# Kernel tuning notes

Measured on AMD Instinct MI355X. Metric: run time of the kernel, lower is better.

## Reference

```python
import jax, jax.numpy as jnp
import numpy as np
from jax import lax

RADIUS = 0.15
K = 32          # num_neighbors
S = 1024        # num_centers
GROUPS = 8      # GroupNorm groups
EPS = 1e-5


def furthest_point_sample(xyz, n_samples):
    # xyz: [B, N, 3] -> indices [B, n_samples] (sequential FPS, start at index 0)
    B, N, _ = xyz.shape
    def step(carry, _):
        min_d, far = carry                      # [B,N], [B]
        sel = jnp.take_along_axis(xyz, far[:, None, None], axis=1)  # [B,1,3]
        d = jnp.sum((xyz - sel) ** 2, axis=-1)  # [B,N]
        min_d = jnp.minimum(min_d, d)
        nxt = jnp.argmax(min_d, axis=-1).astype(jnp.int32)
        return (min_d, nxt), far
    init = (jnp.full((B, N), jnp.inf, dtype=xyz.dtype), jnp.zeros((B,), jnp.int32))
    _, idxs = lax.scan(step, init, None, length=n_samples)  # [n_samples, B]
    return idxs.T  # [B, n_samples]


def ball_query(centers, points, radius, k):
    # centers: [B,3,S], points: [B,3,N] -> neighbor indices [B,S,k]
    B = points.shape[0]
    N = points.shape[-1]
    d2 = jnp.sum((centers[:, :, :, None] - points[:, :, None, :]) ** 2, axis=1)  # [B,S,N]
    valid = d2 < radius * radius
    order = jnp.where(valid, jnp.arange(N, dtype=jnp.int32), jnp.int32(N))
    topk = jnp.sort(order, axis=-1)[..., :k]            # first-k in-ball indices (CUDA ball_query order)
    first = topk[..., :1]
    idx = jnp.where(topk < N, topk, first)              # pad shortfall with first in-ball point
    idx = jnp.where(idx == N, 0, idx)                   # empty ball -> index 0
    return idx


def grouping(x, idx):
    # x: [B,C,N], idx: [B,S,k] -> [B,C,S,k]
    B, C, N = x.shape
    _, s, k = idx.shape
    flat = idx.reshape(B, 1, s * k)
    g = jnp.take_along_axis(x, jnp.broadcast_to(flat, (B, C, s * k)), axis=2)
    return g.reshape(B, C, s, k)


def group_norm(x, gamma, beta):
    # x: [B,C,S,K], GroupNorm(GROUPS)
    B, C, s, k = x.shape
    xg = x.reshape(B, GROUPS, C // GROUPS, s, k)
    mu = jnp.mean(xg, axis=(2, 3, 4), keepdims=True)
    var = jnp.var(xg, axis=(2, 3, 4), keepdims=True)
    xn = ((xg - mu) * lax.rsqrt(var + EPS)).reshape(B, C, s, k)
    return xn * gamma[None, :, None, None] + beta[None, :, None, None]


def mlp_layer(x, w, b, gamma, beta):
    # 1x1 Conv2d + GroupNorm + swish; x: [B,C,S,K], w: [O,C]
    y = jnp.einsum('bcsk,oc->bosk', x, w) + b[None, :, None, None]
    y = group_norm(y, gamma, beta)
    return y * jax.nn.sigmoid(y)


def setup_inputs() -> dict:
    key = jax.random.key(0)
    ks = jax.random.split(key, 20)
    B, C_IN, N = 8, 128, 4096
    features = jax.random.normal(ks[0], (B, C_IN, N), jnp.float32)
    coords = jax.random.uniform(ks[1], (B, 3, N), jnp.float32)
    time_emb = jax.random.normal(ks[2], (B, 64, N), jnp.float32)
    style = jax.random.normal(ks[3], (B, 64), jnp.float32)
    chans = [C_IN + 3, 128, 128, 256]
    inp = dict(features=features, coords=coords, time_emb=time_emb, style=style)
    for i in range(3):
        ci, co = chans[i], chans[i + 1]
        inp[f'w{i+1}'] = jax.random.normal(ks[4 + 4 * i], (co, ci), jnp.float32) / np.sqrt(ci)
        inp[f'b{i+1}'] = jnp.zeros((co,), jnp.float32)
        inp[f'g{i+1}'] = jnp.ones((co,), jnp.float32)
        inp[f'be{i+1}'] = jnp.zeros((co,), jnp.float32)
    return inp


def reference(features, coords, time_emb, style,
              w1, b1, g1, be1, w2, b2, g2, be2, w3, b3, g3, be3):
    # FPS -> center coords
    fps_idx = furthest_point_sample(coords.transpose(0, 2, 1), S)       # [B,S]
    B = coords.shape[0]
    centers = jnp.take_along_axis(coords, jnp.broadcast_to(fps_idx[:, None, :], (B, 3, S)), axis=2)  # [B,3,S]
    # Ball query + grouping (include_coordinates=True)
    nidx = ball_query(centers, coords, RADIUS, K)                       # [B,S,K]
    ncoords = grouping(coords, nidx) - centers[:, :, :, None]           # [B,3,S,K]
    nfeat = jnp.concatenate([ncoords, grouping(features, nidx)], axis=1)  # [B,3+C,S,K]
    # SharedMLP (1x1 conv + GN(8) + swish) x3, then max over neighbors
    x = mlp_layer(nfeat, w1, b1, g1, be1)
    x = mlp_layer(x, w2, b2, g2, be2)
    x = mlp_layer(x, w3, b3, g3, be3)
    out = jnp.max(x, axis=-1)                                           # [B,256,S]
    return out, centers, time_emb[:, :, :S], style
```

## Files before the change

kernel.cpp:

```cpp
#include <hip/hip_runtime.h>
#include <hip/hip_bf16.h>

#define BATCH 8
#define NPTS 4096
#define NS   1024
#define NK   32
#define CIN  128
#define C1PAD 160
#define O1   128
#define O3   256
#define MTOT 32768
#define GN_EPS 1e-5f

typedef float f32x4 __attribute__((ext_vector_type(4)));
typedef float f32x2 __attribute__((ext_vector_type(2)));
typedef short s16x8 __attribute__((ext_vector_type(8)));
typedef short s16x4 __attribute__((ext_vector_type(4)));
typedef unsigned long long u64;
typedef u64 u64x2 __attribute__((ext_vector_type(2)));

static __device__ __forceinline__ unsigned short f2bf(float f){
  unsigned u = __float_as_uint(f);
  u += 0x7fffu + ((u >> 16) & 1u);
  return (unsigned short)(u >> 16);
}
static __device__ __forceinline__ float bf2f(unsigned short h){
  return __uint_as_float(((unsigned)h) << 16);
}
static __device__ __forceinline__ float exact_d2(float ax,float ay,float az,float bx,float by,float bz){
  float dx=__fadd_rn(ax,-bx), dy=__fadd_rn(ay,-by), dz=__fadd_rn(az,-bz);
  return __fadd_rn(__fadd_rn(__fmul_rn(dx,dx),__fmul_rn(dy,dy)),__fmul_rn(dz,dz));
}
static __device__ __forceinline__ unsigned wave_umax_dpp(unsigned v){
  unsigned o;
  o = (unsigned)__builtin_amdgcn_update_dpp(0, (int)v, 0x111, 0xf, 0xf, true); v = (o>v)?o:v;
  o = (unsigned)__builtin_amdgcn_update_dpp(0, (int)v, 0x112, 0xf, 0xf, true); v = (o>v)?o:v;
  o = (unsigned)__builtin_amdgcn_update_dpp(0, (int)v, 0x114, 0xf, 0xf, true); v = (o>v)?o:v;
  o = (unsigned)__builtin_amdgcn_update_dpp(0, (int)v, 0x118, 0xf, 0xf, true); v = (o>v)?o:v;
  o = (unsigned)__builtin_amdgcn_update_dpp(0, (int)v, 0x142, 0xf, 0xf, true); v = (o>v)?o:v;
  o = (unsigned)__builtin_amdgcn_update_dpp(0, (int)v, 0x143, 0xf, 0xf, true); v = (o>v)?o:v;
  return v;
}
static __device__ __forceinline__ float wave_fsum_dpp(float v){
  int o;
  o=__builtin_amdgcn_update_dpp(0,__float_as_int(v),0x111,0xf,0xf,true); v+=__int_as_float(o);
  o=__builtin_amdgcn_update_dpp(0,__float_as_int(v),0x112,0xf,0xf,true); v+=__int_as_float(o);
  o=__builtin_amdgcn_update_dpp(0,__float_as_int(v),0x114,0xf,0xf,true); v+=__int_as_float(o);
  o=__builtin_amdgcn_update_dpp(0,__float_as_int(v),0x118,0xf,0xf,true); v+=__int_as_float(o);
  o=__builtin_amdgcn_update_dpp(0,__float_as_int(v),0x142,0xf,0xf,true); v+=__int_as_float(o);
  o=__builtin_amdgcn_update_dpp(0,__float_as_int(v),0x143,0xf,0xf,true); v+=__int_as_float(o);
  return v;
}
static __device__ __forceinline__ float fast_sigmoid(float x){
  return __builtin_amdgcn_rcpf(1.0f + __expf(-x));
}

#define FPS_BLOCKS 8
#define FT_BASE    8
#define FT_BLOCKS  128
#define ZP_BASE    136
#define ZP_BLOCKS  8
#define WP_BASE    144
#define WP_BLOCKS  36
#define MS_BASE    180
#define MS_BLOCKS  32
#define TOTAL_BLOCKS 212

__global__ __launch_bounds__(256) void k_fused(
    const float* __restrict__ coords, const float* __restrict__ features,
    const float* __restrict__ time_emb, const float* __restrict__ style,
    const float* __restrict__ w1, const float* __restrict__ w2, const float* __restrict__ w3,
    float* __restrict__ centers, float* __restrict__ out_time, float* __restrict__ out_style,
    unsigned short* __restrict__ featT, unsigned short* __restrict__ wfrag,
    float* __restrict__ stats){
  union U {
    struct { float4 lc[NPTS];
             unsigned long long red[2][4] __attribute__((aligned(16))); } fps;
    float tile[64][65];
  };
  __shared__ U sm;
  const int blk = blockIdx.x;
  const int t = threadIdx.x;

  if(blk < FPS_BLOCKS){
    const int b = blk;
    const float* cb = coords + (size_t)b*3*NPTS;
    const int lane = t & 63, wid = t >> 6;
    f32x2 px2[8],py2[8],pz2[8],md2[8];
    #pragma unroll
    for(int i=0;i<8;++i){
      int p0 = t + (2*i)*256;
      px2[i]=(f32x2){cb[p0],cb[p0+256]};
      py2[i]=(f32x2){cb[NPTS+p0],cb[NPTS+p0+256]};
      pz2[i]=(f32x2){cb[2*NPTS+p0],cb[2*NPTS+p0+256]};
      md2[i]=(f32x2){3.4e38f,3.4e38f};
      sm.fps.lc[p0]     = make_float4(px2[i].x, py2[i].x, pz2[i].x, 0.f);
      sm.fps.lc[p0+256] = make_float4(px2[i].y, py2[i].y, pz2[i].y, 0.f);
    }
    float ax=cb[0], ay=cb[NPTS], az=cb[2*NPTS];
    if(t==0){
      centers[(size_t)(b*3+0)*NS]=ax;
      centers[(size_t)(b*3+1)*NS]=ay;
      centers[(size_t)(b*3+2)*NS]=az;
    }
    __syncthreads();
    for(int it=1; it<NS; ++it){
      {
        #pragma clang fp contract(off)
        f32x2 axv={ax,ax}, ayv={ay,ay}, azv={az,az};
        #pragma unroll
        for(int i=0;i<8;++i){
          f32x2 dx=px2[i]-axv, dy=py2[i]-ayv, dz=pz2[i]-azv;
          f32x2 d = dx*dx + dy*dy + dz*dz;
          md2[i].x=fminf(md2[i].x,d.x);
          md2[i].y=fminf(md2[i].y,d.y);
        }
      }
      float m[8];
      #pragma unroll
      for(int i=0;i<8;++i) m[i]=fmaxf(md2[i].x,md2[i].y);
      float bmax=fmaxf(fmaxf(fmaxf(m[0],m[1]),fmaxf(m[2],m[3])),
                       fmaxf(fmaxf(m[4],m[5]),fmaxf(m[6],m[7])));
      unsigned bvb=(unsigned)__builtin_amdgcn_readlane((int)wave_umax_dpp(__float_as_uint(bmax)),63);
      unsigned cand=0u;
      #pragma unroll
      for(int s=15;s>=0;--s){
        float mv = (s&1)? md2[s>>1].y : md2[s>>1].x;
        cand = (__float_as_uint(mv)==bvb) ? ~(unsigned)(s*256+t) : cand;
      }
      unsigned mc = wave_umax_dpp(cand);
      const int buf=it&1;
      if(lane==63) sm.fps.red[buf][wid] = ((u64)bvb<<32) | mc;
      __syncthreads();
      u64x2 r0 = *(const u64x2*)&sm.fps.red[buf][0];
      u64x2 r1 = *(const u64x2*)&sm.fps.red[buf][2];
      u64 a0 = r0.x>r0.y?r0.x:r0.y;
      u64 a1 = r1.x>r1.y?r1.x:r1.y;
      u64 w  = a0>a1?a0:a1;
      unsigned idx = ~(unsigned)w;
      float4 c4 = sm.fps.lc[idx];
      ax=c4.x; ay=c4.y; az=c4.z;
      if(t==0){
        centers[(size_t)(b*3+0)*NS+it]=ax;
        centers[(size_t)(b*3+1)*NS+it]=ay;
        centers[(size_t)(b*3+2)*NS+it]=az;
      }
    }
    return;
  }

  if(blk < ZP_BASE){
    const int pb = blk - FT_BASE;
    for(int j=0;j<8;++j){
      int tid = pb*8 + j;
      int bb = tid>>7, r = tid&127, ct = r>>6, pt = r&63;
      int c0 = ct*64, p0 = pt*64;
      #pragma unroll
      for(int i=0;i<16;++i){
        int c = (t>>6)*16 + i;
        sm.tile[c][t&63] = features[((size_t)bb*CIN + c0 + c)*NPTS + p0 + (t&63)];
      }
      __syncthreads();
      #pragma unroll
      for(int i=0;i<16;++i){
        int pl = (t>>6)*16 + i;
        featT[((size_t)bb*NPTS + p0 + pl)*C1PAD + c0 + (t&63)] = f2bf(sm.tile[t&63][pl]);
      }
      __syncthreads();
    }
    return;
  }

  if(blk < WP_BASE){
    const int zb = blk - ZP_BASE;
    s16x8 z = (s16x8){0,0,0,0,0,0,0,0};
    #pragma unroll 4
    for(int i=0;i<64;++i){
      int q = zb*16384 + i*256 + t;
      int bb = q>>14, rem = q&16383, r = rem>>2, c8 = (rem&3)*8;
      *(s16x8*)&featT[((size_t)bb*NPTS + r)*C1PAD + 128 + c8] = z;
    }
    return;
  }

  if(blk < MS_BASE){
    int task = (blk - WP_BASE)*256 + t;
    if(task >= 9088) return;
    if(task >= 8704){
      int z = task - 8704;
      if(z < 3*BATCH*8*2) stats[z] = 0.f;
      return;
    }
    int layer, of, cs, ln, ncs; size_t base;
    if(task < 2560){ layer=0; ncs=5; base=0;     int r=task;      of=r/320; r%=320; cs=r>>6; ln=r&63; }
    else if(task < 4608){ layer=1; ncs=4; base=20480; int r=task-2560; of=r>>8; r&=255; cs=r>>6; ln=r&63; }
    else { layer=2; ncs=4; base=36864; int r=task-4608; of=r>>8; r&=255; cs=r>>6; ln=r&63; }
    int o = of*16 + (ln&15);
    s16x8 vals;
    #pragma unroll
    for(int i=0;i<8;++i){
      int c = cs*32 + (ln>>4)*8 + i;
      float v = 0.f;
      if(layer==0){
        if(c<128) v = w1[o*131 + c + 3];
        else if(c<131) v = w1[o*131 + (c-128)];
      } else if(layer==1){
        if(c<128) v = w2[o*128 + c];
      } else {
        if(c<128) v = w3[o*128 + c];
      }
      vals[i]=(short)f2bf(v);
    }
    *(s16x8*)&wfrag[base + ((size_t)(of*ncs + cs)*64 + ln)*8] = vals;
    return;
  }

  {
    const int mb = blk - MS_BASE;
    #pragma unroll 4
    for(int i=0;i<16;++i){
      int q = mb*4096 + i*256 + t;
      int f = q*4;
      int bb = f>>16, c = (f>>10)&63, s = f&1023;
      *(float4*)&out_time[f] = *(const float4*)&time_emb[((size_t)bb*64 + c)*NPTS + s];
    }
    if(mb==0){ out_style[t]=style[t]; out_style[256+t]=style[256+t]; }
  }
}

__global__ __launch_bounds__(256) void k_ballq(const float* __restrict__ coords,
                                               const float* __restrict__ centers,
                                               int* __restrict__ nidx){
  const int gw = (blockIdx.x*256 + threadIdx.x) >> 6;
  const int lane = threadIdx.x & 63;
  const int wl = (threadIdx.x >> 6);
  const int b = gw >> 10, s = gw & (NS-1);
  const float* cb = coords + (size_t)b*3*NPTS;
  const float cx = centers[(size_t)(b*3+0)*NS+s];
  const float cy = centers[(size_t)(b*3+1)*NS+s];
  const float cz = centers[(size_t)(b*3+2)*NS+s];
  __shared__ int slots[4][NK];
  int cnt = 0;
  for(int base=0; base<NPTS && cnt<NK; base+=64){
    int p = base + lane;
    float d2 = exact_d2(cb[p], cb[NPTS+p], cb[2*NPTS+p], cx,cy,cz);
    bool valid = d2 < 0.0225f;
    unsigned long long mask = __ballot(valid);
    int pos = cnt + (int)__popcll(mask & ((1ull<<lane)-1ull));
    if(valid && pos < NK) slots[wl][pos] = p;
    cnt += (int)__popcll(mask);
  }
  __syncthreads();
  int first = slots[wl][0];
  if(lane < NK){
    int v = (lane < cnt) ? slots[wl][lane] : first;
    nidx[((size_t)b*NS + s)*NK + lane] = v;
  }
}

__global__ __launch_bounds__(256) void k_gemm1(const unsigned short* __restrict__ featT,
    const int* __restrict__ nidx, const float* __restrict__ coords,
    const float* __restrict__ centers, const unsigned short* __restrict__ wfrag,
    const float* __restrict__ bias, unsigned short* __restrict__ yout,
    float* __restrict__ stats){
  const int b=blockIdx.y, mt=blockIdx.x;
  const int m0=mt*64;
  const int t=threadIdx.x, lane=t&63, wid=t>>6;
  __shared__ unsigned short xs[64][168];
  __shared__ unsigned short ys[64][136];
  __shared__ int pidx[64];
  __shared__ float cenS[2][3];
  __shared__ float wsum[2][8][4];
  if(t<64) pidx[t]=nidx[(size_t)b*MTOT + m0 + t];
  if(t>=64 && t<70){ int u=t-64; int j=u/3, c=u%3; cenS[j][c]=centers[((size_t)b*3+c)*NS + (m0>>5)+j]; }
  __syncthreads();
  for(int q=t;q<1280;q+=256){
    int r=q&63, ch=q>>6;
    *(s16x8*)&xs[r][ch*8] = *(const s16x8*)&featT[((size_t)b*NPTS + pidx[r])*C1PAD + ch*8];
  }
  __syncthreads();
  if(t<64){
    int p=pidx[t]; int sj=t>>5;
    float n0=__fadd_rn(coords[((size_t)b*3+0)*NPTS+p],-cenS[sj][0]);
    float n1=__fadd_rn(coords[((size_t)b*3+1)*NPTS+p],-cenS[sj][1]);
    float n2=__fadd_rn(coords[((size_t)b*3+2)*NPTS+p],-cenS[sj][2]);
    s16x4 nc={(short)f2bf(n0),(short)f2bf(n1),(short)f2bf(n2),0};
    *(s16x4*)&xs[t][128]=nc;
  }
  __syncthreads();
  f32x4 acc[8];
  #pragma unroll
  for(int i=0;i<8;++i) acc[i]=(f32x4){0.f,0.f,0.f,0.f};
  const unsigned short* xrow=&xs[wid*16+(lane&15)][0];
  #pragma unroll
  for(int cs=0;cs<5;++cs){
    s16x8 bfv=*(const s16x8*)&xrow[cs*32+(lane>>4)*8];
    #pragma unroll
    for(int of=0;of<8;++of){
      s16x8 afv=*(const s16x8*)&wfrag[((size_t)(of*5+cs)*64+lane)*8];
      acc[of]=__builtin_amdgcn_mfma_f32_16x16x32_bf16(afv,bfv,acc[of],0,0,0);
    }
  }
  #pragma unroll
  for(int of=0;of<8;++of){
    float ls=0.f,lq=0.f;
    int obase=of*16+((lane>>4)<<2);
    #pragma unroll
    for(int r=0;r<4;++r){
      float y=acc[of][r]+bias[obase+r];
      ys[wid*16+(lane&15)][obase+r]=f2bf(y);
      ls+=y; lq+=y*y;
    }
    ls=wave_fsum_dpp(ls); lq=wave_fsum_dpp(lq);
    if(lane==63){ wsum[0][of][wid]=ls; wsum[1][of][wid]=lq; }
  }
  __syncthreads();
  for(int q=t;q<1024;q+=256){
    int r=q&63, ch=q>>6;
    *(s16x8*)&yout[((size_t)b*MTOT+m0+r)*O1 + ch*8] = *(const s16x8*)&ys[r][ch*8];
  }
  if(t<8){
    float s1v=wsum[0][t][0]+wsum[0][t][1]+wsum[0][t][2]+wsum[0][t][3];
    float s2v=wsum[1][t][0]+wsum[1][t][1]+wsum[1][t][2]+wsum[1][t][3];
    atomicAdd(&stats[((0*BATCH+b)*8+t)*2+0],s1v);
    atomicAdd(&stats[((0*BATCH+b)*8+t)*2+1],s2v);
  }
}

template<int LAYER>
__global__ __launch_bounds__(256) void k_gemm23(const unsigned short* __restrict__ xin,
    const unsigned short* __restrict__ wfrag, const float* __restrict__ bias,
    const float* __restrict__ stats, const float* __restrict__ gprev,
    const float* __restrict__ beprev, unsigned short* __restrict__ yout,
    float* __restrict__ ymm, float* __restrict__ statsOut){
  const int b=blockIdx.y, mt=blockIdx.x;
  const int m0=mt*64;
  const int t=threadIdx.x, lane=t&63, wid=t>>6;
  __shared__ unsigned short xs[64][136];
  __shared__ unsigned short ys[64][136];
  __shared__ float lsc[CIN], lsh[CIN];
  __shared__ float wsum[2][8][4];
  if(t<CIN){
    int g = t>>4;
    const float cnt = 16.0f*NS*NK;
    float s1=stats[(((LAYER-1)*BATCH+b)*8+g)*2+0];
    float s2=stats[(((LAYER-1)*BATCH+b)*8+g)*2+1];
    float mu=s1/cnt, var=s2/cnt-mu*mu;
    float sc=gprev[t]*rsqrtf(var+GN_EPS);
    lsc[t]=sc; lsh[t]=beprev[t]-mu*sc;
  }
  __syncthreads();
  for(int q=t;q<1024;q+=256){
    int r=q&63, ch=q>>6;
    s16x8 v = *(const s16x8*)&xin[((size_t)b*MTOT + m0 + r)*CIN + ch*8];
    s16x8 o;
    #pragma unroll
    for(int i=0;i<8;++i){
      int c=ch*8+i;
      float x = bf2f((unsigned short)v[i]);
      x = x*lsc[c] + lsh[c];
      o[i]=(short)f2bf(x*fast_sigmoid(x));
    }
    *(s16x8*)&xs[r][ch*8]=o;
  }
  __syncthreads();
  const unsigned short* xrow=&xs[wid*16+(lane&15)][0];
  s16x8 bfv[4];
  #pragma unroll
  for(int cs=0;cs<4;++cs) bfv[cs]=*(const s16x8*)&xrow[cs*32+(lane>>4)*8];
  const int NPH=(LAYER==2)?2:1;
  #pragma unroll
  for(int ph=0; ph<NPH; ++ph){
    f32x4 acc[8];
    #pragma unroll
    for(int i=0;i<8;++i) acc[i]=(f32x4){0.f,0.f,0.f,0.f};
    #pragma unroll
    for(int cs=0;cs<4;++cs){
      #pragma unroll
      for(int of=0;of<8;++of){
        int ofg=ph*8+of;
        s16x8 afv=*(const s16x8*)&wfrag[((size_t)(ofg*4+cs)*64+lane)*8];
        acc[of]=__builtin_amdgcn_mfma_f32_16x16x32_bf16(afv,bfv[cs],acc[of],0,0,0);
      }
    }
    #pragma unroll
    for(int of=0;of<8;++of){
      float ls=0.f,lq=0.f;
      int lobase=of*16+((lane>>4)<<2);
      #pragma unroll
      for(int r=0;r<4;++r){
        float y=acc[of][r]+bias[ph*128+lobase+r];
        ys[wid*16+(lane&15)][lobase+r]=f2bf(y);
        ls+=y; lq+=y*y;
      }
      ls=wave_fsum_dpp(ls); lq=wave_fsum_dpp(lq);
      if(lane==63){ wsum[0][of][wid]=ls; wsum[1][of][wid]=lq; }
    }
    __syncthreads();
    if constexpr(LAYER==1){
      for(int q=t;q<1024;q+=256){
        int r=q&63, ch=q>>6;
        *(s16x8*)&yout[((size_t)b*MTOT+m0+r)*O1 + ch*8] = *(const s16x8*)&ys[r][ch*8];
      }
    } else {
      int c = t&127, sg = t>>7;
      float mn=3.4e38f, mx=-3.4e38f;
      #pragma unroll 8
      for(int k=0;k<32;++k){
        float v = bf2f(ys[sg*32+k][c]);
        mn=fminf(mn,v); mx=fmaxf(mx,v);
      }
      *(float2*)&ymm[(((size_t)b*NS + mt*2 + sg)*512) + (size_t)(ph*128+c)*2] = make_float2(mn,mx);
    }
    if(t<8){
      float s1v=wsum[0][t][0]+wsum[0][t][1]+wsum[0][t][2]+wsum[0][t][3];
      float s2v=wsum[1][t][0]+wsum[1][t][1]+wsum[1][t][2]+wsum[1][t][3];
      int g = (LAYER==2) ? (ph*4 + (t>>1)) : t;
      atomicAdd(&statsOut[((LAYER*BATCH+b)*8+g)*2+0],s1v);
      atomicAdd(&statsOut[((LAYER*BATCH+b)*8+g)*2+1],s2v);
    }
    if(ph+1<NPH) __syncthreads();
  }
}

__global__ __launch_bounds__(256) void k_out(const float* __restrict__ ymm,
    const float* __restrict__ stats, const float* __restrict__ g3,
    const float* __restrict__ be3, float* __restrict__ out){
  const int b=blockIdx.z, st=blockIdx.x;
  const int t=threadIdx.x;
  __shared__ float outT[256][33];
  const int c=t, g=c>>5;
  const float cnt = 32.0f*NS*NK;
  float s1=stats[((2*BATCH+b)*8+g)*2+0];
  float s2=stats[((2*BATCH+b)*8+g)*2+1];
  float mu=s1/cnt, var=s2/cnt-mu*mu;
  float sc=g3[c]*rsqrtf(var+GN_EPS);
  float sh=be3[c]-mu*sc;
  for(int si=0;si<32;++si){
    int s=st*32+si;
    float2 v=*(const float2*)&ymm[((size_t)b*NS+s)*512 + (size_t)c*2];
    float za=v.x*sc+sh, zb=v.y*sc+sh;
    float fa=za*fast_sigmoid(za);
    float fb=zb*fast_sigmoid(zb);
    outT[c][si]=fmaxf(fa,fb);
  }
  __syncthreads();
  #pragma unroll
  for(int i=0;i<32;++i){
    int row=(t>>5)+i*8;
    out[((size_t)(b*256+row))*NS + st*32 + (t&31)] = outT[row][t&31];
  }
}

extern "C" void kernel_launch(void* const* d_in, const int* in_sizes, int n_in,
                              void* d_out, int out_size, void* d_ws, size_t ws_size,
                              hipStream_t stream){
  const float* features=(const float*)d_in[0];
  const float* coords=(const float*)d_in[1];
  const float* time_emb=(const float*)d_in[2];
  const float* style=(const float*)d_in[3];
  const float* w1=(const float*)d_in[4];
  const float* b1=(const float*)d_in[5];
  const float* g1=(const float*)d_in[6];
  const float* be1=(const float*)d_in[7];
  const float* w2=(const float*)d_in[8];
  const float* b2=(const float*)d_in[9];
  const float* g2=(const float*)d_in[10];
  const float* be2=(const float*)d_in[11];
  const float* w3=(const float*)d_in[12];
  const float* b3=(const float*)d_in[13];
  const float* g3=(const float*)d_in[14];
  const float* be3=(const float*)d_in[15];

  float* out0=(float*)d_out;
  float* out_centers=out0 + (size_t)BATCH*O3*NS;
  float* out_time=out_centers + (size_t)BATCH*3*NS;
  float* out_style=out_time + (size_t)BATCH*64*NS;

  char* ws=(char*)d_ws;
  int* nidx=(int*)(ws + 131072);
  unsigned short* featT=(unsigned short*)(ws + 1179648);
  unsigned short* wfrag=(unsigned short*)(ws + 11796480);
  float* stats=(float*)(ws + 11939840);
  float* ymm=(float*)(ws + 12582912);
  unsigned short* y1=(unsigned short*)(ws + 33554432);
  unsigned short* y2=(unsigned short*)(ws + 100663296);

  k_fused<<<TOTAL_BLOCKS,256,0,stream>>>(coords,features,time_emb,style,w1,w2,w3,
                                         out_centers,out_time,out_style,featT,wfrag,stats);
  k_ballq<<<2048,256,0,stream>>>(coords,out_centers,nidx);
  k_gemm1<<<dim3(512,BATCH),256,0,stream>>>(featT,nidx,coords,out_centers,wfrag,b1,y1,stats);
  k_gemm23<1><<<dim3(512,BATCH),256,0,stream>>>(y1,wfrag+20480,b2,stats,g1,be1,y2,ymm,stats);
  k_gemm23<2><<<dim3(512,BATCH),256,0,stream>>>(y2,wfrag+36864,b3,stats,g2,be2,y2,ymm,stats);
  k_out<<<dim3(32,1,BATCH),256,0,stream>>>(ymm,stats,g3,be3,out0);
}
```

Baseline: 1.051 ms.

## Process two batches per FPS block to share per-iteration barrier latency

Each furthest-point-sampling block now handles two batch elements at once, which halves the FPS block count. The two independent dependency chains are interleaved in a single iteration loop with one __syncthreads. The aim is to hide the latency of the serial reduce-and-barrier chain by giving each wave twice the independent work. The cost is twice the registers and LDS per block and roughly double the ALU work per iteration, so each FPS block may run longer.

```diff
diff --git a/kernel.cpp b/kernel.cpp
--- a/kernel.cpp
+++ b/kernel.cpp
@@ -55,16 +55,16 @@
   return __builtin_amdgcn_rcpf(1.0f + __expf(-x));
 }
 
-#define FPS_BLOCKS 8
-#define FT_BASE    8
+#define FPS_BLOCKS 4
+#define FT_BASE    4
 #define FT_BLOCKS  128
-#define ZP_BASE    136
+#define ZP_BASE    132
 #define ZP_BLOCKS  8
-#define WP_BASE    144
+#define WP_BASE    140
 #define WP_BLOCKS  36
-#define MS_BASE    180
+#define MS_BASE    176
 #define MS_BLOCKS  32
-#define TOTAL_BLOCKS 212
+#define TOTAL_BLOCKS 208
 
 __global__ __launch_bounds__(256) void k_fused(
     const float* __restrict__ coords, const float* __restrict__ features,
@@ -74,8 +74,9 @@
     unsigned short* __restrict__ featT, unsigned short* __restrict__ wfrag,
     float* __restrict__ stats){
   union U {
-    struct { float4 lc[NPTS];
-             unsigned long long red[2][4] __attribute__((aligned(16))); } fps;
+    struct { float4 lcA[NPTS]; float4 lcB[NPTS];
+             unsigned long long redA[2][4] __attribute__((aligned(16)));
+             unsigned long long redB[2][4] __attribute__((aligned(16))); } fps;
     float tile[64][65];
   };
   __shared__ U sm;
@@ -83,67 +84,107 @@
   const int t = threadIdx.x;
 
   if(blk < FPS_BLOCKS){
-    const int b = blk;
-    const float* cb = coords + (size_t)b*3*NPTS;
+    const int bA = blk*2, bB = blk*2+1;
+    const float* cbA = coords + (size_t)bA*3*NPTS;
+    const float* cbB = coords + (size_t)bB*3*NPTS;
     const int lane = t & 63, wid = t >> 6;
-    f32x2 px2[8],py2[8],pz2[8],md2[8];
+    f32x2 pxA[8],pyA[8],pzA[8],mdA[8];
+    f32x2 pxB[8],pyB[8],pzB[8],mdB[8];
     #pragma unroll
     for(int i=0;i<8;++i){
       int p0 = t + (2*i)*256;
-      px2[i]=(f32x2){cb[p0],cb[p0+256]};
-      py2[i]=(f32x2){cb[NPTS+p0],cb[NPTS+p0+256]};
-      pz2[i]=(f32x2){cb[2*NPTS+p0],cb[2*NPTS+p0+256]};
-      md2[i]=(f32x2){3.4e38f,3.4e38f};
-      sm.fps.lc[p0]     = make_float4(px2[i].x, py2[i].x, pz2[i].x, 0.f);
-      sm.fps.lc[p0+256] = make_float4(px2[i].y, py2[i].y, pz2[i].y, 0.f);
-    }
-    float ax=cb[0], ay=cb[NPTS], az=cb[2*NPTS];
+      pxA[i]=(f32x2){cbA[p0],cbA[p0+256]};
+      pyA[i]=(f32x2){cbA[NPTS+p0],cbA[NPTS+p0+256]};
+      pzA[i]=(f32x2){cbA[2*NPTS+p0],cbA[2*NPTS+p0+256]};
+      pxB[i]=(f32x2){cbB[p0],cbB[p0+256]};
+      pyB[i]=(f32x2){cbB[NPTS+p0],cbB[NPTS+p0+256]};
+      pzB[i]=(f32x2){cbB[2*NPTS+p0],cbB[2*NPTS+p0+256]};
+      mdA[i]=(f32x2){3.4e38f,3.4e38f};
+      mdB[i]=(f32x2){3.4e38f,3.4e38f};
+      sm.fps.lcA[p0]     = make_float4(pxA[i].x, pyA[i].x, pzA[i].x, 0.f);
+      sm.fps.lcA[p0+256] = make_float4(pxA[i].y, pyA[i].y, pzA[i].y, 0.f);
+      sm.fps.lcB[p0]     = make_float4(pxB[i].x, pyB[i].x, pzB[i].x, 0.f);
+      sm.fps.lcB[p0+256] = make_float4(pxB[i].y, pyB[i].y, pzB[i].y, 0.f);
+    }
+    float axA=cbA[0], ayA=cbA[NPTS], azA=cbA[2*NPTS];
+    float axB=cbB[0], ayB=cbB[NPTS], azB=cbB[2*NPTS];
     if(t==0){
-      centers[(size_t)(b*3+0)*NS]=ax;
-      centers[(size_t)(b*3+1)*NS]=ay;
-      centers[(size_t)(b*3+2)*NS]=az;
+      centers[(size_t)(bA*3+0)*NS]=axA;
+      centers[(size_t)(bA*3+1)*NS]=ayA;
+      centers[(size_t)(bA*3+2)*NS]=azA;
+    } else if(t==1){
+      centers[(size_t)(bB*3+0)*NS]=axB;
+      centers[(size_t)(bB*3+1)*NS]=ayB;
+      centers[(size_t)(bB*3+2)*NS]=azB;
     }
     __syncthreads();
     for(int it=1; it<NS; ++it){
       {
         #pragma clang fp contract(off)
-        f32x2 axv={ax,ax}, ayv={ay,ay}, azv={az,az};
+        f32x2 axvA={axA,axA}, ayvA={ayA,ayA}, azvA={azA,azA};
+        f32x2 axvB={axB,axB}, ayvB={ayB,ayB}, azvB={azB,azB};
         #pragma unroll
         for(int i=0;i<8;++i){
-          f32x2 dx=px2[i]-axv, dy=py2[i]-ayv, dz=pz2[i]-azv;
-          f32x2 d = dx*dx + dy*dy + dz*dz;
-          md2[i].x=fminf(md2[i].x,d.x);
-          md2[i].y=fminf(md2[i].y,d.y);
+          f32x2 dxA=pxA[i]-axvA, dyA=pyA[i]-ayvA, dzA=pzA[i]-azvA;
+          f32x2 dA = dxA*dxA + dyA*dyA + dzA*dzA;
+          mdA[i]=__builtin_elementwise_min(mdA[i],dA);
+          f32x2 dxB=pxB[i]-axvB, dyB=pyB[i]-ayvB, dzB=pzB[i]-azvB;
+          f32x2 dB = dxB*dxB + dyB*dyB + dzB*dzB;
+          mdB[i]=__builtin_elementwise_min(mdB[i],dB);
         }
       }
-      float m[8];
-      #pragma unroll
-      for(int i=0;i<8;++i) m[i]=fmaxf(md2[i].x,md2[i].y);
-      float bmax=fmaxf(fmaxf(fmaxf(m[0],m[1]),fmaxf(m[2],m[3])),
-                       fmaxf(fmaxf(m[4],m[5]),fmaxf(m[6],m[7])));
-      unsigned bvb=(unsigned)__builtin_amdgcn_readlane((int)wave_umax_dpp(__float_as_uint(bmax)),63);
-      unsigned cand=0u;
+      f32x2 tA=__builtin_elementwise_max(
+                 __builtin_elementwise_max(__builtin_elementwise_max(mdA[0],mdA[1]),
+                                           __builtin_elementwise_max(mdA[2],mdA[3])),
+                 __builtin_elementwise_max(__builtin_elementwise_max(mdA[4],mdA[5]),
+                                           __builtin_elementwise_max(mdA[6],mdA[7])));
+      f32x2 tB=__builtin_elementwise_max(
+                 __builtin_elementwise_max(__builtin_elementwise_max(mdB[0],mdB[1]),
+                                           __builtin_elementwise_max(mdB[2],mdB[3])),
+                 __builtin_elementwise_max(__builtin_elementwise_max(mdB[4],mdB[5]),
+                                           __builtin_elementwise_max(mdB[6],mdB[7])));
+      float bmaxA=fmaxf(tA.x,tA.y), bmaxB=fmaxf(tB.x,tB.y);
+      unsigned bvbA=(unsigned)__builtin_amdgcn_readlane((int)wave_umax_dpp(__float_as_uint(bmaxA)),63);
+      unsigned bvbB=(unsigned)__builtin_amdgcn_readlane((int)wave_umax_dpp(__float_as_uint(bmaxB)),63);
+      unsigned candA=0u, candB=0u;
       #pragma unroll
       for(int s=15;s>=0;--s){
-        float mv = (s&1)? md2[s>>1].y : md2[s>>1].x;
-        cand = (__float_as_uint(mv)==bvb) ? ~(unsigned)(s*256+t) : cand;
-      }
-      unsigned mc = wave_umax_dpp(cand);
+        float mvA = (s&1)? mdA[s>>1].y : mdA[s>>1].x;
+        candA = (__float_as_uint(mvA)==bvbA) ? ~(unsigned)(s*256+t) : candA;
+        float mvB = (s&1)? mdB[s>>1].y : mdB[s>>1].x;
+        candB = (__float_as_uint(mvB)==bvbB) ? ~(unsigned)(s*256+t) : candB;
+      }
+      unsigned mcA = wave_umax_dpp(candA);
+      unsigned mcB = wave_umax_dpp(candB);
       const int buf=it&1;
-      if(lane==63) sm.fps.red[buf][wid] = ((u64)bvb<<32) | mc;
+      if(lane==63){
+        sm.fps.redA[buf][wid] = ((u64)bvbA<<32) | mcA;
+        sm.fps.redB[buf][wid] = ((u64)bvbB<<32) | mcB;
+      }
       __syncthreads();
-      u64x2 r0 = *(const u64x2*)&sm.fps.red[buf][0];
-      u64x2 r1 = *(const u64x2*)&sm.fps.red[buf][2];
-      u64 a0 = r0.x>r0.y?r0.x:r0.y;
-      u64 a1 = r1.x>r1.y?r1.x:r1.y;
-      u64 w  = a0>a1?a0:a1;
-      unsigned idx = ~(unsigned)w;
-      float4 c4 = sm.fps.lc[idx];
-      ax=c4.x; ay=c4.y; az=c4.z;
+      u64x2 rA0 = *(const u64x2*)&sm.fps.redA[buf][0];
+      u64x2 rA1 = *(const u64x2*)&sm.fps.redA[buf][2];
+      u64x2 rB0 = *(const u64x2*)&sm.fps.redB[buf][0];
+      u64x2 rB1 = *(const u64x2*)&sm.fps.redB[buf][2];
+      u64 aA0 = rA0.x>rA0.y?rA0.x:rA0.y;
+      u64 aA1 = rA1.x>rA1.y?rA1.x:rA1.y;
+      u64 wA  = aA0>aA1?aA0:aA1;
+      u64 aB0 = rB0.x>rB0.y?rB0.x:rB0.y;
+      u64 aB1 = rB1.x>rB1.y?rB1.x:rB1.y;
+      u64 wB  = aB0>aB1?aB0:aB1;
+      unsigned idxA = ~(unsigned)wA, idxB = ~(unsigned)wB;
+      float4 cA = sm.fps.lcA[idxA];
+      float4 cB = sm.fps.lcB[idxB];
+      axA=cA.x; ayA=cA.y; azA=cA.z;
+      axB=cB.x; ayB=cB.y; azB=cB.z;
       if(t==0){
-        centers[(size_t)(b*3+0)*NS+it]=ax;
-        centers[(size_t)(b*3+1)*NS+it]=ay;
-        centers[(size_t)(b*3+2)*NS+it]=az;
+        centers[(size_t)(bA*3+0)*NS+it]=axA;
+        centers[(size_t)(bA*3+1)*NS+it]=ayA;
+        centers[(size_t)(bA*3+2)*NS+it]=azA;
+      } else if(t==1){
+        centers[(size_t)(bB*3+0)*NS+it]=axB;
+        centers[(size_t)(bB*3+1)*NS+it]=ayB;
+        centers[(size_t)(bB*3+2)*NS+it]=azB;
       }
     }
     return;
```

Measured after the change: 1.501 ms. 1.43x slower.
